# Performance work log

Measured on AMD Instinct MI355X. Metric: run time of the kernel, lower is better.

Reference implementation:

```python
import jax, jax.numpy as jnp
import numpy as np

B_, L_, D_MODEL, D_STATE, EXPAND, D_CONV = 4, 2048, 1024, 16, 2, 4
D_INNER = EXPAND * D_MODEL          # 2048
DT_RANK = (D_MODEL + 15) // 16      # 64


def setup_inputs() -> dict:
    key = jax.random.key(0)
    ks = jax.random.split(key, 8)
    s = lambda k, shape, scale: jax.random.normal(k, shape, jnp.float32) * scale
    return {
        "u": jax.random.normal(ks[0], (B_, L_, D_MODEL), jnp.float32),
        "hiddens": jnp.zeros((B_, D_INNER, D_STATE), jnp.float32),  # initial SSM state h0
        "in_proj_w": s(ks[1], (D_MODEL, 2 * D_INNER), D_MODEL ** -0.5),
        "conv_w": s(ks[2], (D_INNER, 1, D_CONV), D_CONV ** -0.5),   # depthwise kernel (O,I/g,K)
        "conv_b": jnp.zeros((D_INNER,), jnp.float32),
        "x_proj_w": s(ks[3], (D_INNER, DT_RANK + 2 * D_STATE), D_INNER ** -0.5),
        "dt_proj_w": s(ks[4], (DT_RANK, D_INNER), DT_RANK ** -0.5),
        "dt_proj_b": jnp.log(jnp.expm1(jnp.full((D_INNER,), 0.01, jnp.float32))),  # softplus^-1(0.01)
        "A_log": jnp.log(jnp.tile(jnp.arange(1, D_STATE + 1, dtype=jnp.float32), (D_INNER, 1))),
        "D": jnp.ones((D_INNER,), jnp.float32),
        "out_proj_w": s(ks[5], (D_INNER, D_MODEL), D_INNER ** -0.5),
        "training": 0,
    }


def reference(u, hiddens, in_proj_w, conv_w, conv_b, x_proj_w, dt_proj_w,
              dt_proj_b, A_log, D, out_proj_w, training):
    # --- input projection -> (x, res) ---
    x, res = jnp.split(u @ in_proj_w, 2, axis=-1)           # each [b, l, d_inner]

    # --- depthwise causal conv1d (width D_CONV) + silu ---
    xc = jax.lax.conv_general_dilated(
        x.transpose(0, 2, 1), conv_w, (1,), [(D_CONV - 1, 0)],
        dimension_numbers=('NCH', 'OIH', 'NCH'), feature_group_count=D_INNER)
    x = jax.nn.silu((xc + conv_b[None, :, None]).transpose(0, 2, 1))  # [b, l, d_inner]

    # --- data-dependent SSM parameters ---
    dbc = x @ x_proj_w                                       # [b, l, dt_rank + 2n]
    delta = jax.nn.softplus(dbc[..., :DT_RANK] @ dt_proj_w + dt_proj_b)  # [b, l, d_inner]
    Bm = dbc[..., DT_RANK:DT_RANK + D_STATE]                 # [b, l, n]
    Cm = dbc[..., DT_RANK + D_STATE:]                        # [b, l, n]
    A = -jnp.exp(A_log)                                      # [d_inner, n]

    # --- selective scan over time ---
    def step(h, inp):
        dt, Bt, Ct, ut = inp                                 # [b,d], [b,n], [b,n], [b,d]
        dA = jnp.exp(dt[:, :, None] * A)                     # [b, d, n]
        h = dA * h + dt[:, :, None] * Bt[:, None, :] * ut[:, :, None]
        y = jnp.einsum('bdn,bn->bd', h, Ct)
        return h, y

    xs = (delta.transpose(1, 0, 2), Bm.transpose(1, 0, 2),
          Cm.transpose(1, 0, 2), x.transpose(1, 0, 2))
    _, ys = jax.lax.scan(step, hiddens, xs)                  # ys: [l, b, d_inner]

    y = ys.transpose(1, 0, 2) + x * D                        # skip via D
    y = y * jax.nn.silu(res)                                 # gated output
    return y @ out_proj_w                                    # [b, l, d_model]
```

## Files before the change

### kernel.cpp

```cpp
#include <hip/hip_runtime.h>
#include <hip/hip_bf16.h>
#include <cstddef>

#define B_   4
#define L_   2048
#define DM   1024
#define DI   2048
#define NST  16
#define DTR  64
#define NBC  96
#define NTOK 8192

using bf16 = __hip_bfloat16;
typedef __attribute__((ext_vector_type(8))) short bf16x8;
typedef __attribute__((ext_vector_type(4))) short s16x4;
typedef __attribute__((ext_vector_type(4))) float f32x4;

__device__ __forceinline__ float bf2f(short s) {
  unsigned u = ((unsigned)(unsigned short)s) << 16;
  float f; __builtin_memcpy(&f, &u, 4); return f;
}
__device__ __forceinline__ short f2bs(float f) {
  __hip_bfloat16 h = __float2bfloat16(f);
  short s; __builtin_memcpy(&s, &h, 2); return s;
}
__device__ __forceinline__ float sigmoidf_fast(float x) {
  return 1.f / (1.f + __expf(-x));
}

#define GLD16(g, l) __builtin_amdgcn_global_load_lds( \
  (const __attribute__((address_space(1))) unsigned int*)(g), \
  (__attribute__((address_space(3))) unsigned int*)(l), 16, 0, 0)

__device__ __forceinline__ float swz_xor8(float x) {
  return __builtin_bit_cast(float,
    __builtin_amdgcn_ds_swizzle(__builtin_bit_cast(int, x), 0x201F));
}
__device__ __forceinline__ float swz_xor4(float x) {
  return __builtin_bit_cast(float,
    __builtin_amdgcn_ds_swizzle(__builtin_bit_cast(int, x), 0x101F));
}
template<int CTRL>
__device__ __forceinline__ float qperm(float x) {
  return __builtin_bit_cast(float,
    __builtin_amdgcn_update_dpp(0, __builtin_bit_cast(int, x), CTRL, 0xf, 0xf, false));
}
template<int S>
__device__ __forceinline__ float swz_bcast16(float x) {
  return __builtin_bit_cast(float,
    __builtin_amdgcn_ds_swizzle(__builtin_bit_cast(int, x), (S << 5) | 0x10));
}

__global__ __launch_bounds__(256)
void cvt_f2b(const float* __restrict__ in, short* __restrict__ out)
{
  const size_t i = ((size_t)blockIdx.x * 256 + threadIdx.x) * 8;
  float4 a0 = *(const float4*)(in + i);
  float4 a1 = *(const float4*)(in + i + 4);
  union { bf16x8 v; short h[8]; } o;
  o.h[0] = f2bs(a0.x); o.h[1] = f2bs(a0.y); o.h[2] = f2bs(a0.z); o.h[3] = f2bs(a0.w);
  o.h[4] = f2bs(a1.x); o.h[5] = f2bs(a1.y); o.h[6] = f2bs(a1.z); o.h[7] = f2bs(a1.w);
  *(bf16x8*)(out + i) = o.v;
}

__global__ __launch_bounds__(256)
void transpose_f2b(const float* __restrict__ in, short* __restrict__ out,
                   int R, int Cc, int lin, int lout)
{
  __shared__ short t[32][33];
  const int r0 = blockIdx.x * 32, c0 = blockIdx.y * 32;
  const int tx = threadIdx.x, ty = threadIdx.y;
#pragma unroll
  for (int i = 0; i < 4; i++) {
    int r = r0 + ty + i * 8;
    int c = c0 + tx;
    short v = 0;
    if (r < R && c < Cc) v = f2bs(in[(size_t)r * lin + c]);
    t[ty + i * 8][tx] = v;
  }
  __syncthreads();
#pragma unroll
  for (int i = 0; i < 4; i++) {
    int c = c0 + ty + i * 8;
    int r = r0 + tx;
    if (c < Cc && r < lout) out[(size_t)c * lout + r] = t[tx][ty + i * 8];
  }
}

__global__ __launch_bounds__(256)
void gemm_bt(const short* __restrict__ A, const short* __restrict__ Bt,
             void* __restrict__ Cv, void* __restrict__ Cv2, const float* __restrict__ bias,
             int N, int K, int lda, int ldb, int ldc, int ldc2, int mode)
{
  __shared__ short As[128][32];
  __shared__ short Bs[128][32];
  const int gx = gridDim.x;
  const int nwg = gx * gridDim.y;
  const int lid = blockIdx.x + gx * blockIdx.y;
  const int cpx = nwg >> 3;
  const int swz = (lid & 7) * cpx + (lid >> 3);
  const int m0 = (swz % gx) * 128;
  const int n0 = (swz / gx) * 128;
  const int tid  = threadIdx.x;
  const int wave = tid >> 6, lane = tid & 63;
  const int wr = (wave >> 1) * 64, wc = (wave & 1) * 64;
  const int la = lane & 15, gq = lane >> 4;
  f32x4 acc[4][4] = {};

  for (int k0 = 0; k0 < K; k0 += 32) {
#pragma unroll
    for (int i = 0; i < 2; i++) {
      int idx = tid + i * 256;
      int row = idx >> 2, kc = (idx & 3) * 8;
      GLD16(A  + (size_t)(m0 + row) * lda + k0 + kc, &As[row][kc]);
      GLD16(Bt + (size_t)(n0 + row) * ldb + k0 + kc, &Bs[row][kc]);
    }
    __syncthreads();
    bf16x8 af[4], bfr[4];
#pragma unroll
    for (int i = 0; i < 4; i++) af[i]  = *(const bf16x8*)(&As[wr + i * 16 + la][gq * 8]);
#pragma unroll
    for (int j = 0; j < 4; j++) bfr[j] = *(const bf16x8*)(&Bs[wc + j * 16 + la][gq * 8]);
#pragma unroll
    for (int i = 0; i < 4; i++)
#pragma unroll
      for (int j = 0; j < 4; j++)
        acc[i][j] = __builtin_amdgcn_mfma_f32_16x16x32_bf16(af[i], bfr[j], acc[i][j], 0, 0, 0);
    __syncthreads();
  }

#pragma unroll
  for (int i = 0; i < 4; i++) {
    int rowb = m0 + wr + i * 16 + gq * 4;
#pragma unroll
    for (int j = 0; j < 4; j++) {
      int col = n0 + wc + j * 16 + la;
      if (col >= N) continue;
      if (mode == 2) {
#pragma unroll
        for (int r = 0; r < 4; r++)
          ((float*)Cv)[(size_t)(rowb + r) * ldc + col] = acc[i][j][r];
      } else if (mode == 4) {
        if (col < DTR) {
#pragma unroll
          for (int r = 0; r < 4; r++)
            ((short*)Cv)[(size_t)(rowb + r) * ldc + col] = f2bs(acc[i][j][r]);
        } else {
          s16x4 pk;
#pragma unroll
          for (int r = 0; r < 4; r++) pk[r] = f2bs(acc[i][j][r]);
          *(s16x4*)((short*)Cv2 + (size_t)(col - DTR) * ldc2 + rowb) = pk;
        }
      } else if (mode == 5) {
        short* base = (col < DI) ? (short*)Cv : (short*)Cv2;
        int c = (col < DI) ? col : col - DI;
        int ld = (col < DI) ? ldc : ldc2;
#pragma unroll
        for (int r = 0; r < 4; r++)
          base[(size_t)(rowb + r) * ld + c] = f2bs(acc[i][j][r]);
      } else if (mode == 6) {
#pragma unroll
        for (int r = 0; r < 4; r++) {
          float v = acc[i][j][r] + bias[rowb + r];
          float e = exp2f(v * 1.44269504f);
          v = (v > 20.f) ? v : 0.69314718f * __log2f(1.f + e);
          ((short*)Cv)[(size_t)(rowb + r) * ldc + col] = f2bs(v);
        }
      } else {
#pragma unroll
        for (int r = 0; r < 4; r++)
          ((short*)Cv)[(size_t)(rowb + r) * ldc + col] = f2bs(acc[i][j][r]);
      }
    }
  }
}

__global__ __launch_bounds__(256)
void conv_silu(const short* __restrict__ xb, const float* __restrict__ cw,
               const float* __restrict__ cb, short* __restrict__ xs)
{
  const int token = blockIdx.x;
  const int l = token & (L_ - 1);
  const int d0 = threadIdx.x * 8;

  float w[32];
#pragma unroll
  for (int i = 0; i < 8; i++) {
    float4 t = *(const float4*)(cw + (size_t)(d0 + i) * 4);
    w[i * 4 + 0] = t.x; w[i * 4 + 1] = t.y; w[i * 4 + 2] = t.z; w[i * 4 + 3] = t.w;
  }
  float acc[8];
  {
    float4 b0 = *(const float4*)(cb + d0);
    float4 b1 = *(const float4*)(cb + d0 + 4);
    acc[0] = b0.x; acc[1] = b0.y; acc[2] = b0.z; acc[3] = b0.w;
    acc[4] = b1.x; acc[5] = b1.y; acc[6] = b1.z; acc[7] = b1.w;
  }
#pragma unroll
  for (int j = 0; j < 4; j++) {
    int lj = l - 3 + j;
    if (lj >= 0) {
      bf16x8 xv = *(const bf16x8*)(xb + (size_t)(token - 3 + j) * DI + d0);
#pragma unroll
      for (int i = 0; i < 8; i++) acc[i] += w[i * 4 + j] * bf2f(xv[i]);
    }
  }
  union { bf16x8 v; short h[8]; } o;
#pragma unroll
  for (int i = 0; i < 8; i++) {
    float v = acc[i];
    o.h[i] = f2bs(v * sigmoidf_fast(v));
  }
  *(bf16x8*)(xs + (size_t)token * DI + d0) = o.v;
}

__global__ __launch_bounds__(256, 2)
void scan_kernel(const short* __restrict__ dT, const short* __restrict__ dbcT,
                 const short* __restrict__ xs, short* __restrict__ resy,
                 const float* __restrict__ A_log, const float* __restrict__ Dw,
                 const float* __restrict__ h0)
{
  const int lane = threadIdx.x & 63;
  const int grp = threadIdx.x >> 4, n = threadIdx.x & 15;
  const int ch = blockIdx.x * 16 + grp;
  const int b = ch >> 11, d = ch & (DI - 1);
  const bool b3 = (lane & 8) != 0, b2 = (lane & 4) != 0,
             b1 = (lane & 2) != 0, b0 = (lane & 1) != 0;
  const float An2 = -__expf(A_log[d * NST + n]) * 1.44269504f;
  const float Dd = Dw[d];
  float h = h0[(size_t)ch * NST + n];

  const size_t t0 = (size_t)b * L_;
  const short* dRow = dT   + (size_t)d * NTOK + t0;
  const short* bRow = dbcT + (size_t)n * NTOK + t0;
  const short* cRow = bRow + (size_t)NST * NTOK;
  const short* uLn  = xs   + (t0 + n) * DI + d;
  short*       yCol = resy + (t0 + n) * DI + d;

  auto LOADB = [&](int lv, bf16x8& t0v, bf16x8& t1v, bf16x8& B0v, bf16x8& B1v,
                   bf16x8& C0v, bf16x8& C1v, short& uo, short& rr) {
    t0v = *(const bf16x8*)(dRow + lv);
    t1v = *(const bf16x8*)(dRow + lv + 8);
    B0v = *(const bf16x8*)(bRow + lv);
    B1v = *(const bf16x8*)(bRow + lv + 8);
    C0v = *(const bf16x8*)(cRow + lv);
    C1v = *(const bf16x8*)(cRow + lv + 8);
    uo = uLn[(size_t)lv * DI];
    rr = yCol[(size_t)lv * DI];
  };

  auto STEP = [&](int lv, bf16x8 t0v, bf16x8 t1v, bf16x8 B0v, bf16x8 B1v,
                  bf16x8 C0v, bf16x8 C1v, short uo, short rr) {
    const float uown = bf2f(uo);
    float uf[16];
    uf[0]  = swz_bcast16<0>(uown);   uf[1]  = swz_bcast16<1>(uown);
    uf[2]  = swz_bcast16<2>(uown);   uf[3]  = swz_bcast16<3>(uown);
    uf[4]  = swz_bcast16<4>(uown);   uf[5]  = swz_bcast16<5>(uown);
    uf[6]  = swz_bcast16<6>(uown);   uf[7]  = swz_bcast16<7>(uown);
    uf[8]  = swz_bcast16<8>(uown);   uf[9]  = swz_bcast16<9>(uown);
    uf[10] = swz_bcast16<10>(uown);  uf[11] = swz_bcast16<11>(uown);
    uf[12] = swz_bcast16<12>(uown);  uf[13] = swz_bcast16<13>(uown);
    uf[14] = swz_bcast16<14>(uown);  uf[15] = swz_bcast16<15>(uown);
    float dA[16], w[16];
#pragma unroll
    for (int s = 0; s < 16; s++) {
      float dt = bf2f(s < 8 ? t0v[s] : t1v[s - 8]);
      dA[s] = exp2f(dt * An2);
      w[s]  = dt * uf[s] * bf2f(s < 8 ? B0v[s] : B1v[s - 8]);
    }
    float p[16];
#pragma unroll
    for (int s = 0; s < 16; s++) {
      h = __builtin_fmaf(dA[s], h, w[s]);
      p[s] = h * bf2f(s < 8 ? C0v[s] : C1v[s - 8]);
    }
    float q8[8];
#pragma unroll
    for (int i = 0; i < 8; i++) {
      float keep = b3 ? p[i + 8] : p[i];
      float send = b3 ? p[i]     : p[i + 8];
      q8[i] = keep + swz_xor8(send);
    }
    float q4[4];
#pragma unroll
    for (int i = 0; i < 4; i++) {
      float keep = b2 ? q8[i + 4] : q8[i];
      float send = b2 ? q8[i]     : q8[i + 4];
      q4[i] = keep + swz_xor4(send);
    }
    float q2[2];
#pragma unroll
    for (int i = 0; i < 2; i++) {
      float keep = b1 ? q4[i + 2] : q4[i];
      float send = b1 ? q4[i]     : q4[i + 2];
      q2[i] = keep + qperm<0x4E>(send);
    }
    float keep = b0 ? q2[1] : q2[0];
    float send = b0 ? q2[0] : q2[1];
    float ysum = keep + qperm<0xB1>(send);
    ysum = __builtin_fmaf(uown, Dd, ysum);
    float r = bf2f(rr);
    float yv = ysum * (r * sigmoidf_fast(r));
    yCol[(size_t)lv * DI] = f2bs(yv);
  };

  bf16x8 a0, a1, a2, a3, a4, a5; short ua, ra;
  bf16x8 c0, c1, c2, c3, c4, c5; short ub, rb;
  LOADB(0, a0, a1, a2, a3, a4, a5, ua, ra);
  for (int l = 0; l < L_; l += 32) {
    LOADB(l + 16, c0, c1, c2, c3, c4, c5, ub, rb);
    STEP(l, a0, a1, a2, a3, a4, a5, ua, ra);
    if (l + 32 < L_) LOADB(l + 32, a0, a1, a2, a3, a4, a5, ua, ra);
    STEP(l + 16, c0, c1, c2, c3, c4, c5, ub, rb);
  }
}

extern "C" void kernel_launch(void* const* d_in, const int* in_sizes, int n_in,
                              void* d_out, int out_size, void* d_ws, size_t ws_size,
                              hipStream_t stream)
{
  const float* u        = (const float*)d_in[0];
  const float* hiddens  = (const float*)d_in[1];
  const float* in_proj  = (const float*)d_in[2];
  const float* conv_w   = (const float*)d_in[3];
  const float* conv_b   = (const float*)d_in[4];
  const float* x_proj   = (const float*)d_in[5];
  const float* dt_proj  = (const float*)d_in[6];
  const float* dt_bias  = (const float*)d_in[7];
  const float* A_log    = (const float*)d_in[8];
  const float* Dw       = (const float*)d_in[9];
  const float* out_proj = (const float*)d_in[10];
  float* out = (float*)d_out;

  char* w = (char*)d_ws;
  short* Wt1  = (short*)w;
  short* Wt4  = Wt1;
  w += (size_t)4096 * 1024 * 2;
  short* Wxp  = (short*)w; w += (size_t)128  * 2048 * 2;
  short* dtw  = (short*)w; w += (size_t)2048 * 64   * 2;
  short* xbuf = (short*)w; w += (size_t)NTOK * DI   * 2;
  short* resy = (short*)w; w += (size_t)NTOK * DI   * 2;
  short* dbc  = (short*)w; w += (size_t)NTOK * DTR  * 2;
  short* dbcT = (short*)w; w += (size_t)32   * NTOK * 2;
  short* ub   = (short*)d_out;
  short* xs   = (short*)d_out;
  short* dT   = xbuf;

  dim3 tb(32, 8);
  cvt_f2b<<<4096, 256, 0, stream>>>(u, ub);
  transpose_f2b<<<dim3(32, 128), tb, 0, stream>>>(in_proj,  Wt1, 1024, 4096, 4096, 1024);
  transpose_f2b<<<dim3(64, 3),   tb, 0, stream>>>(x_proj,   Wxp, 2048, 96,   96,   2048);
  transpose_f2b<<<dim3(2, 64),   tb, 0, stream>>>(dt_proj,  dtw, 64,   2048, 2048, 64);

  gemm_bt<<<dim3(64, 32), 256, 0, stream>>>(ub, Wt1, xbuf, resy, nullptr,
                                            4096, 1024, 1024, 1024, DI, DI, 5);
  transpose_f2b<<<dim3(64, 32),  tb, 0, stream>>>(out_proj, Wt4, 2048, 1024, 1024, 2048);
  conv_silu<<<NTOK, 256, 0, stream>>>(xbuf, conv_w, conv_b, xs);
  gemm_bt<<<dim3(64, 1), 256, 0, stream>>>(xs, Wxp, dbc, dbcT, nullptr,
                                           96, 2048, 2048, 2048, DTR, NTOK, 4);
  gemm_bt<<<dim3(16, 64), 256, 0, stream>>>(dtw, dbc, dT, nullptr, dt_bias,
                                            NTOK, 64, 64, 64, NTOK, 0, 6);
  scan_kernel<<<512, 256, 0, stream>>>(dT, dbcT, xs, resy, A_log, Dw, hiddens);
  gemm_bt<<<dim3(64, 8), 256, 0, stream>>>(resy, Wt4, out, nullptr, nullptr,
                                           1024, 2048, 2048, 2048, 1024, 0, 2);
}
```

Measured before the change: 646.0 us.

## Deepen GEMM K-tile to 64 with XOR-swizzled LDS and fuse prep kernels

The bf16 MFMA GEMM now stages 64-wide K slices per iteration instead of 32. This halves the number of barrier pairs per K loop. Global loads are placed into LDS with an XOR swizzle on row&7, and fragment reads apply the matching XOR, to avoid LDS bank conflicts on the wider rows. Separately, the input cast and three weight transposes are merged into a single `prep` launch to cut launch overhead. LDS use per block doubles, which may reduce occupancy.

```diff
diff --git a/kernel.cpp b/kernel.cpp
--- a/kernel.cpp
+++ b/kernel.cpp
@@ -51,25 +51,12 @@
     __builtin_amdgcn_ds_swizzle(__builtin_bit_cast(int, x), (S << 5) | 0x10));
 }
 
-__global__ __launch_bounds__(256)
-void cvt_f2b(const float* __restrict__ in, short* __restrict__ out)
-{
-  const size_t i = ((size_t)blockIdx.x * 256 + threadIdx.x) * 8;
-  float4 a0 = *(const float4*)(in + i);
-  float4 a1 = *(const float4*)(in + i + 4);
-  union { bf16x8 v; short h[8]; } o;
-  o.h[0] = f2bs(a0.x); o.h[1] = f2bs(a0.y); o.h[2] = f2bs(a0.z); o.h[3] = f2bs(a0.w);
-  o.h[4] = f2bs(a1.x); o.h[5] = f2bs(a1.y); o.h[6] = f2bs(a1.z); o.h[7] = f2bs(a1.w);
-  *(bf16x8*)(out + i) = o.v;
-}
-
-__global__ __launch_bounds__(256)
-void transpose_f2b(const float* __restrict__ in, short* __restrict__ out,
-                   int R, int Cc, int lin, int lout)
-{
-  __shared__ short t[32][33];
-  const int r0 = blockIdx.x * 32, c0 = blockIdx.y * 32;
-  const int tx = threadIdx.x, ty = threadIdx.y;
+__device__ __forceinline__ void transpose_tile(
+    const float* __restrict__ in, short* __restrict__ out,
+    int R, int Cc, int lin, int lout, int bx, int by, int tid, short (*t)[33])
+{
+  const int r0 = bx * 32, c0 = by * 32;
+  const int tx = tid & 31, ty = tid >> 5;
 #pragma unroll
   for (int i = 0; i < 4; i++) {
     int r = r0 + ty + i * 8;
@@ -88,12 +75,54 @@
 }
 
 __global__ __launch_bounds__(256)
+void prep(const float* __restrict__ u, short* __restrict__ ub,
+          const float* __restrict__ in_proj, short* __restrict__ Wt1,
+          const float* __restrict__ x_proj, short* __restrict__ Wxp,
+          const float* __restrict__ dt_proj, short* __restrict__ dtw)
+{
+  __shared__ short t[32][33];
+  int id = blockIdx.x;
+  const int tid = threadIdx.x;
+  if (id < 4096) {
+    const size_t i = ((size_t)id * 256 + tid) * 8;
+    float4 a0 = *(const float4*)(u + i);
+    float4 a1 = *(const float4*)(u + i + 4);
+    union { bf16x8 v; short h[8]; } o;
+    o.h[0] = f2bs(a0.x); o.h[1] = f2bs(a0.y); o.h[2] = f2bs(a0.z); o.h[3] = f2bs(a0.w);
+    o.h[4] = f2bs(a1.x); o.h[5] = f2bs(a1.y); o.h[6] = f2bs(a1.z); o.h[7] = f2bs(a1.w);
+    *(bf16x8*)(ub + i) = o.v;
+    return;
+  }
+  id -= 4096;
+  if (id < 4096) {
+    transpose_tile(in_proj, Wt1, 1024, 4096, 4096, 1024, id & 31, id >> 5, tid, t);
+    return;
+  }
+  id -= 4096;
+  if (id < 192) {
+    transpose_tile(x_proj, Wxp, 2048, 96, 96, 2048, id % 64, id / 64, tid, t);
+    return;
+  }
+  id -= 192;
+  transpose_tile(dt_proj, dtw, 64, 2048, 2048, 64, id & 1, id >> 1, tid, t);
+}
+
+__global__ __launch_bounds__(256)
+void transpose_f2b(const float* __restrict__ in, short* __restrict__ out,
+                   int R, int Cc, int lin, int lout)
+{
+  __shared__ short t[32][33];
+  transpose_tile(in, out, R, Cc, lin, lout, blockIdx.x, blockIdx.y,
+                 threadIdx.x + threadIdx.y * 32, t);
+}
+
+__global__ __launch_bounds__(256)
 void gemm_bt(const short* __restrict__ A, const short* __restrict__ Bt,
              void* __restrict__ Cv, void* __restrict__ Cv2, const float* __restrict__ bias,
              int N, int K, int lda, int ldb, int ldc, int ldc2, int mode)
 {
-  __shared__ short As[128][32];
-  __shared__ short Bs[128][32];
+  __shared__ short As[128][64];
+  __shared__ short Bs[128][64];
   const int gx = gridDim.x;
   const int nwg = gx * gridDim.y;
   const int lid = blockIdx.x + gx * blockIdx.y;
@@ -105,27 +134,33 @@
   const int wave = tid >> 6, lane = tid & 63;
   const int wr = (wave >> 1) * 64, wc = (wave & 1) * 64;
   const int la = lane & 15, gq = lane >> 4;
+  const int rs = (la & 7) << 3;
   f32x4 acc[4][4] = {};
 
-  for (int k0 = 0; k0 < K; k0 += 32) {
-#pragma unroll
-    for (int i = 0; i < 2; i++) {
+  for (int k0 = 0; k0 < K; k0 += 64) {
+#pragma unroll
+    for (int i = 0; i < 4; i++) {
       int idx = tid + i * 256;
-      int row = idx >> 2, kc = (idx & 3) * 8;
-      GLD16(A  + (size_t)(m0 + row) * lda + k0 + kc, &As[row][kc]);
-      GLD16(Bt + (size_t)(n0 + row) * ldb + k0 + kc, &Bs[row][kc]);
+      int row = idx >> 3, kc = (idx & 7) * 8;
+      int kcs = kc ^ ((row & 7) << 3);
+      GLD16(A  + (size_t)(m0 + row) * lda + k0 + kcs, &As[row][kc]);
+      GLD16(Bt + (size_t)(n0 + row) * ldb + k0 + kcs, &Bs[row][kc]);
     }
     __syncthreads();
-    bf16x8 af[4], bfr[4];
-#pragma unroll
-    for (int i = 0; i < 4; i++) af[i]  = *(const bf16x8*)(&As[wr + i * 16 + la][gq * 8]);
-#pragma unroll
-    for (int j = 0; j < 4; j++) bfr[j] = *(const bf16x8*)(&Bs[wc + j * 16 + la][gq * 8]);
-#pragma unroll
-    for (int i = 0; i < 4; i++)
-#pragma unroll
-      for (int j = 0; j < 4; j++)
-        acc[i][j] = __builtin_amdgcn_mfma_f32_16x16x32_bf16(af[i], bfr[j], acc[i][j], 0, 0, 0);
+#pragma unroll
+    for (int kk = 0; kk < 2; kk++) {
+      const int cl = (kk * 32 + gq * 8) ^ rs;
+      bf16x8 af[4], bfr[4];
+#pragma unroll
+      for (int i = 0; i < 4; i++) af[i]  = *(const bf16x8*)(&As[wr + i * 16 + la][cl]);
+#pragma unroll
+      for (int j = 0; j < 4; j++) bfr[j] = *(const bf16x8*)(&Bs[wc + j * 16 + la][cl]);
+#pragma unroll
+      for (int i = 0; i < 4; i++)
+#pragma unroll
+        for (int j = 0; j < 4; j++)
+          acc[i][j] = __builtin_amdgcn_mfma_f32_16x16x32_bf16(af[i], bfr[j], acc[i][j], 0, 0, 0);
+    }
     __syncthreads();
   }
 
@@ -346,15 +381,12 @@
   short* xs   = (short*)d_out;
   short* dT   = xbuf;
 
-  dim3 tb(32, 8);
-  cvt_f2b<<<4096, 256, 0, stream>>>(u, ub);
-  transpose_f2b<<<dim3(32, 128), tb, 0, stream>>>(in_proj,  Wt1, 1024, 4096, 4096, 1024);
-  transpose_f2b<<<dim3(64, 3),   tb, 0, stream>>>(x_proj,   Wxp, 2048, 96,   96,   2048);
-  transpose_f2b<<<dim3(2, 64),   tb, 0, stream>>>(dt_proj,  dtw, 64,   2048, 2048, 64);
+  prep<<<4096 + 4096 + 192 + 128, 256, 0, stream>>>(u, ub, in_proj, Wt1,
+                                                    x_proj, Wxp, dt_proj, dtw);
 
   gemm_bt<<<dim3(64, 32), 256, 0, stream>>>(ub, Wt1, xbuf, resy, nullptr,
                                             4096, 1024, 1024, 1024, DI, DI, 5);
-  transpose_f2b<<<dim3(64, 32),  tb, 0, stream>>>(out_proj, Wt4, 2048, 1024, 1024, 2048);
+  transpose_f2b<<<dim3(64, 32), dim3(32, 8), 0, stream>>>(out_proj, Wt4, 2048, 1024, 1024, 2048);
   conv_silu<<<NTOK, 256, 0, stream>>>(xbuf, conv_w, conv_b, xs);
   gemm_bt<<<dim3(64, 1), 256, 0, stream>>>(xs, Wxp, dbc, dbcT, nullptr,
                                            96, 2048, 2048, 2048, DTR, NTOK, 4);
```

Measured after the change: 617.2 us. 4.5% less time.
